# Kernel optimization log

Measured on AMD Instinct MI355X. Metric: run time of the kernel, lower is better.

The kernel has to match this reference:

```python
import jax, jax.numpy as jnp
import numpy as np

VOCAB = 10000
HID = 256
BATCH = 32
STEPS = 256


def setup_inputs() -> dict:
    key = jax.random.key(0)
    k1, k2, k3, k4 = jax.random.split(key, 4)
    # glorot-uniform style scaling
    s_xh = np.sqrt(6.0 / (VOCAB + HID)).astype(np.float32)
    s_hh = np.sqrt(6.0 / (HID + HID)).astype(np.float32)
    s_d = np.sqrt(6.0 / (HID + VOCAB)).astype(np.float32)
    return {
        "tokens": jax.random.randint(k1, (BATCH, STEPS), 0, VOCAB, dtype=jnp.int32),
        "W_xh": jax.random.uniform(k2, (VOCAB, HID), jnp.float32, -s_xh, s_xh),
        "W_hh": jax.random.uniform(k3, (HID, HID), jnp.float32, -s_hh, s_hh),
        "b_h": jnp.zeros((HID,), jnp.float32),
        "W_d": jax.random.uniform(k4, (HID, VOCAB), jnp.float32, -s_d, s_d),
        "b_d": jnp.zeros((VOCAB,), jnp.float32),
        "h0": jnp.zeros((BATCH, HID), jnp.float32),
    }


def reference(tokens, W_xh, W_hh, b_h, W_d, b_d, h0):
    # call(): X = one_hot(transpose(tokens), vocab)  -> time-major [T, B, V]
    # one_hot(x) @ W_xh is exactly a row gather from W_xh (same math, efficient form)
    xw = W_xh[jnp.transpose(tokens)]  # [T, B, H]

    # SimpleRNNCell: h_t = tanh(x_t @ W_xh + h_{t-1} @ W_hh + b)
    def step(h, xt):
        h_new = jnp.tanh(xt + h @ W_hh + b_h)
        return h_new, h_new

    state, Y = jax.lax.scan(step, h0, xw)  # Y: [T, B, H], state: [B, H]

    # Dense over flattened sequence outputs -> [T*B, vocab]
    output = Y.reshape(-1, Y.shape[-1]) @ W_d + b_d
    return output, state
```

## Files before the change

### kernel.cpp

```cpp
#include <hip/hip_runtime.h>
#include <hip/hip_bf16.h>

#define VOCAB 10000
#define HID 256
#define BATCH 32
#define STEPS 256
#define MROWS (STEPS * BATCH)

typedef __bf16 bf16x8 __attribute__((ext_vector_type(8)));
typedef float f32x4 __attribute__((ext_vector_type(4)));

template <int CTRL>
static __device__ __forceinline__ float dpp_add(float s) {
    int t = __builtin_amdgcn_update_dpp(
        0, __builtin_bit_cast(int, s), CTRL, 0xf, 0xf, true);
    return s + __builtin_bit_cast(float, t);
}
#define DPP_XOR1 0xB1
#define DPP_XOR2 0x4E

static __device__ __forceinline__ float swz4_add(float s) {
    int t = __builtin_amdgcn_ds_swizzle(__builtin_bit_cast(int, s), 0x101F);
    return s + __builtin_bit_cast(float, t);
}

__global__ void transpose_wd_kernel(const float* __restrict__ Wd,
                                    __hip_bfloat16* __restrict__ WdT) {
    __shared__ __hip_bfloat16 tile[64][68];
    const int n0 = blockIdx.x * 64;
    const int k0 = blockIdx.y * 64;
    const int tid = threadIdx.x;
    const int lane = tid & 63;
    const int w = tid >> 6;

#pragma unroll
    for (int i = 0; i < 16; ++i) {
        int k = w * 16 + i;
        int n = lane;
        float v = (n0 + n < VOCAB) ? Wd[(size_t)(k0 + k) * VOCAB + n0 + n] : 0.f;
        tile[n][k] = __float2bfloat16(v);
    }
    __syncthreads();
#pragma unroll
    for (int i = 0; i < 16; ++i) {
        int n = w * 16 + i;
        int k = lane;
        if (n0 + n < VOCAB)
            WdT[(size_t)(n0 + n) * HID + k0 + k] = tile[n][k];
    }
}

#define HSEG 36

__global__ __launch_bounds__(1024)
__attribute__((amdgpu_waves_per_eu(4, 4)))
void rnn_kernel(const int* __restrict__ tokens, const float* __restrict__ Wxh,
                const float* __restrict__ Whh, const float* __restrict__ bh,
                const float* __restrict__ h0, __hip_bfloat16* __restrict__ ybf,
                float* __restrict__ state_out) {
    const int b = blockIdx.x;
    const int tid = threadIdx.x;
    const int cg = tid >> 3;
    const int q = tid & 7;
    const int c0 = cg * 2;

    __shared__ alignas(16) float hseg[2][8][HSEG];

    float w0[32], w1[32];
    {
        const float* wp = Whh + (size_t)(q * 32) * HID + c0;
#pragma unroll
        for (int i = 0; i < 32; ++i) {
            w0[i] = wp[(size_t)i * HID];
            w1[i] = wp[(size_t)i * HID + 1];
        }
    }

    const float bj0 = bh[c0];
    const float bj1 = bh[c0 + 1];
    const int* trow = tokens + b * STEPS;

    if (q == 0) {
        hseg[0][c0 >> 5][c0 & 31] = h0[b * HID + c0];
        hseg[0][c0 >> 5][(c0 & 31) + 1] = h0[b * HID + c0 + 1];
    }

    float2 xv = *reinterpret_cast<const float2*>(&Wxh[(size_t)trow[0] * HID + c0]);
    __syncthreads();

    float hn0 = 0.f, hn1 = 0.f;
    int cur = 0;
    for (int t = 0; t < STEPS; ++t) {
#pragma unroll
        for (int i = 0; i < 32; ++i) {
            asm volatile("" : "+v"(w0[i]), "+v"(w1[i]));
        }

        int ti = (t + 1 < STEPS) ? t + 1 : STEPS - 1;
        float2 xn = *reinterpret_cast<const float2*>(
            &Wxh[(size_t)trow[ti] * HID + c0]);

        const float* hb = &hseg[cur][q][0];
        float s0 = 0.f, s1 = 0.f;
#pragma unroll
        for (int j4 = 0; j4 < 8; ++j4) {
            float4 hv = *reinterpret_cast<const float4*>(&hb[j4 * 4]);
            s0 += hv.x * w0[j4 * 4 + 0] + hv.y * w0[j4 * 4 + 1] +
                  hv.z * w0[j4 * 4 + 2] + hv.w * w0[j4 * 4 + 3];
            s1 += hv.x * w1[j4 * 4 + 0] + hv.y * w1[j4 * 4 + 1] +
                  hv.z * w1[j4 * 4 + 2] + hv.w * w1[j4 * 4 + 3];
        }
        s0 = dpp_add<DPP_XOR1>(s0);  s1 = dpp_add<DPP_XOR1>(s1);
        s0 = dpp_add<DPP_XOR2>(s0);  s1 = dpp_add<DPP_XOR2>(s1);
        s0 = swz4_add(s0);           s1 = swz4_add(s1);

        float z0 = xv.x + bj0 + s0;
        float z1 = xv.y + bj1 + s1;
        float e0 = __expf(2.f * z0);
        float e1 = __expf(2.f * z1);
        hn0 = 1.f - 2.f / (e0 + 1.f);
        hn1 = 1.f - 2.f / (e1 + 1.f);

        if (q == 0) {
            float2 hp = make_float2(hn0, hn1);
            *reinterpret_cast<float2*>(&hseg[cur ^ 1][c0 >> 5][c0 & 31]) = hp;
        } else if (q == 1) {
            __hip_bfloat162 yp;
            yp.x = __float2bfloat16(hn0);
            yp.y = __float2bfloat16(hn1);
            *reinterpret_cast<__hip_bfloat162*>(
                &ybf[(size_t)t * (BATCH * HID) + b * HID + c0]) = yp;
        }

        __syncthreads();
        cur ^= 1;
        xv = xn;
    }
    if (q == 1) {
        state_out[b * HID + c0] = hn0;
        state_out[b * HID + c0 + 1] = hn1;
    }
}

__global__ __launch_bounds__(256)
void gemm_kernel(const __hip_bfloat16* __restrict__ A,
                 const __hip_bfloat16* __restrict__ BT,
                 const float* __restrict__ bd,
                 float* __restrict__ C) {
    const int m0 = blockIdx.x * 128;
    const int n0 = blockIdx.y * 128;
    const int tid = threadIdx.x;
    const int lane = tid & 63;
    const int wv = tid >> 6;
    const int wr = wv >> 1;
    const int wc = wv & 1;
    const int r15 = lane & 15;
    const int g = lane >> 4;

    __shared__ alignas(16) __hip_bfloat16 As[128][264];

#pragma unroll
    for (int c = 0; c < 16; ++c) {
        int chunk = c * 256 + tid;
        int row = chunk >> 5;
        int cc = chunk & 31;
        bf16x8 av = *reinterpret_cast<const bf16x8*>(
            &A[(size_t)(m0 + row) * HID + cc * 8]);
        *reinterpret_cast<bf16x8*>(&As[row][cc * 8]) = av;
    }
    __syncthreads();

    const __hip_bfloat16* brow[4];
    bool bok[4];
#pragma unroll
    for (int n = 0; n < 4; ++n) {
        int rn = n0 + wc * 64 + n * 16 + r15;
        bok[n] = rn < VOCAB;
        brow[n] = BT + (size_t)(bok[n] ? rn : 0) * HID;
    }
    bf16x8 bzero;
#pragma unroll
    for (int e = 0; e < 8; ++e) bzero[e] = (__bf16)0.f;

    f32x4 acc[4][4] = {};
    bf16x8 bcur[4];
#pragma unroll
    for (int n = 0; n < 4; ++n)
        bcur[n] = bok[n] ? *reinterpret_cast<const bf16x8*>(&brow[n][g * 8])
                         : bzero;

    for (int kk8 = 0; kk8 < 8; ++kk8) {
        bf16x8 bnext[4];
        if (kk8 < 7) {
            int off = (kk8 + 1) * 32 + g * 8;
#pragma unroll
            for (int n = 0; n < 4; ++n)
                bnext[n] = bok[n]
                    ? *reinterpret_cast<const bf16x8*>(&brow[n][off])
                    : bzero;
        }
        bf16x8 af[4];
#pragma unroll
        for (int m = 0; m < 4; ++m)
            af[m] = *reinterpret_cast<const bf16x8*>(
                &As[wr * 64 + m * 16 + r15][kk8 * 32 + g * 8]);
#pragma unroll
        for (int m = 0; m < 4; ++m)
#pragma unroll
            for (int n = 0; n < 4; ++n)
                acc[m][n] = __builtin_amdgcn_mfma_f32_16x16x32_bf16(
                    bcur[n], af[m], acc[m][n], 0, 0, 0);
        if (kk8 < 7) {
#pragma unroll
            for (int n = 0; n < 4; ++n) bcur[n] = bnext[n];
        }
    }

#pragma unroll
    for (int m = 0; m < 4; ++m) {
        int row = m0 + wr * 64 + m * 16 + r15;
#pragma unroll
        for (int n = 0; n < 4; ++n) {
            int cb = n0 + wc * 64 + n * 16;
            if (cb + 15 < VOCAB) {
                int col = cb + g * 4;
                float4 bv = *reinterpret_cast<const float4*>(&bd[col]);
                f32x4 v = acc[m][n];
                v[0] += bv.x; v[1] += bv.y; v[2] += bv.z; v[3] += bv.w;
                *reinterpret_cast<f32x4*>(&C[(size_t)row * VOCAB + col]) = v;
            }
        }
    }
}

extern "C" void kernel_launch(void* const* d_in, const int* in_sizes, int n_in,
                              void* d_out, int out_size, void* d_ws, size_t ws_size,
                              hipStream_t stream) {
    const int* tokens  = (const int*)d_in[0];
    const float* Wxh   = (const float*)d_in[1];
    const float* Whh   = (const float*)d_in[2];
    const float* bh    = (const float*)d_in[3];
    const float* Wd    = (const float*)d_in[4];
    const float* bd    = (const float*)d_in[5];
    const float* h0    = (const float*)d_in[6];

    float* out = (float*)d_out;
    float* state_out = out + (size_t)MROWS * VOCAB;

    __hip_bfloat16* ybf = (__hip_bfloat16*)d_ws;
    __hip_bfloat16* wdt = (__hip_bfloat16*)((char*)d_ws + (size_t)MROWS * HID * 2);

    hipLaunchKernelGGL(transpose_wd_kernel, dim3(157, 4), dim3(256), 0, stream,
                       Wd, wdt);
    hipLaunchKernelGGL(rnn_kernel, dim3(BATCH), dim3(1024), 0, stream,
                       tokens, Wxh, Whh, bh, h0, ybf, state_out);
    hipLaunchKernelGGL(gemm_kernel, dim3(64, 79), dim3(256), 0, stream,
                       ybf, wdt, bd, out);
}
```

Baseline: 429.5 us.

## Halve RNN block to 512 threads with four columns per thread group

The recurrent kernel now runs 512 threads per batch row, each 8-lane group owning four hidden columns instead of two, so each thread holds 128 weight registers. A new kernel transposes W_hh into the workspace so those weights load as contiguous float4 rows. The intent is to cut the per-step barrier cost and the number of waves that synchronise, at the price of more FMA work per thread, higher register pressure, and an extra kernel launch.

```diff
diff --git a/kernel.cpp b/kernel.cpp
--- a/kernel.cpp
+++ b/kernel.cpp
@@ -9,6 +9,7 @@
 
 typedef __bf16 bf16x8 __attribute__((ext_vector_type(8)));
 typedef float f32x4 __attribute__((ext_vector_type(4)));
+typedef unsigned short u16x4 __attribute__((ext_vector_type(4)));
 
 template <int CTRL>
 static __device__ __forceinline__ float dpp_add(float s) {
@@ -50,95 +51,123 @@
     }
 }
 
+__global__ void transpose_whh_kernel(const float* __restrict__ Whh,
+                                     float* __restrict__ WhhT) {
+    __shared__ float tile[64][65];
+    const int j0 = blockIdx.x * 64;
+    const int k0 = blockIdx.y * 64;
+    const int tid = threadIdx.x;
+    const int lane = tid & 63;
+    const int w = tid >> 6;
+
+#pragma unroll
+    for (int i = 0; i < 16; ++i) {
+        int k = w * 16 + i;
+        tile[lane][k] = Whh[(size_t)(k0 + k) * HID + j0 + lane];
+    }
+    __syncthreads();
+#pragma unroll
+    for (int i = 0; i < 16; ++i) {
+        int j = w * 16 + i;
+        WhhT[(size_t)(j0 + j) * HID + k0 + lane] = tile[j][lane];
+    }
+}
+
 #define HSEG 36
 
-__global__ __launch_bounds__(1024)
-__attribute__((amdgpu_waves_per_eu(4, 4)))
+__global__ __launch_bounds__(512, 2)
+__attribute__((amdgpu_waves_per_eu(2, 2)))
 void rnn_kernel(const int* __restrict__ tokens, const float* __restrict__ Wxh,
-                const float* __restrict__ Whh, const float* __restrict__ bh,
+                const float* __restrict__ WhhT, const float* __restrict__ bh,
                 const float* __restrict__ h0, __hip_bfloat16* __restrict__ ybf,
                 float* __restrict__ state_out) {
     const int b = blockIdx.x;
     const int tid = threadIdx.x;
     const int cg = tid >> 3;
     const int q = tid & 7;
-    const int c0 = cg * 2;
+    const int c0 = cg * 4;
 
     __shared__ alignas(16) float hseg[2][8][HSEG];
 
-    float w0[32], w1[32];
-    {
-        const float* wp = Whh + (size_t)(q * 32) * HID + c0;
-#pragma unroll
-        for (int i = 0; i < 32; ++i) {
-            w0[i] = wp[(size_t)i * HID];
-            w1[i] = wp[(size_t)i * HID + 1];
-        }
-    }
-
-    const float bj0 = bh[c0];
-    const float bj1 = bh[c0 + 1];
+    float w[4][32];
+#pragma unroll
+    for (int c = 0; c < 4; ++c) {
+        const float4* wp = reinterpret_cast<const float4*>(
+            WhhT + (size_t)(c0 + c) * HID + q * 32);
+#pragma unroll
+        for (int i4 = 0; i4 < 8; ++i4) {
+            float4 v = wp[i4];
+            w[c][i4 * 4 + 0] = v.x;
+            w[c][i4 * 4 + 1] = v.y;
+            w[c][i4 * 4 + 2] = v.z;
+            w[c][i4 * 4 + 3] = v.w;
+        }
+    }
+
+    const float4 bj = *reinterpret_cast<const float4*>(&bh[c0]);
     const int* trow = tokens + b * STEPS;
 
     if (q == 0) {
-        hseg[0][c0 >> 5][c0 & 31] = h0[b * HID + c0];
-        hseg[0][c0 >> 5][(c0 & 31) + 1] = h0[b * HID + c0 + 1];
-    }
-
-    float2 xv = *reinterpret_cast<const float2*>(&Wxh[(size_t)trow[0] * HID + c0]);
-    __syncthreads();
-
-    float hn0 = 0.f, hn1 = 0.f;
+        *reinterpret_cast<float4*>(&hseg[0][c0 >> 5][c0 & 31]) =
+            *reinterpret_cast<const float4*>(&h0[b * HID + c0]);
+    }
+
+    float4 xv = *reinterpret_cast<const float4*>(&Wxh[(size_t)trow[0] * HID + c0]);
+    __syncthreads();
+
+    float hn[4] = {0.f, 0.f, 0.f, 0.f};
     int cur = 0;
     for (int t = 0; t < STEPS; ++t) {
-#pragma unroll
-        for (int i = 0; i < 32; ++i) {
-            asm volatile("" : "+v"(w0[i]), "+v"(w1[i]));
-        }
-
         int ti = (t + 1 < STEPS) ? t + 1 : STEPS - 1;
-        float2 xn = *reinterpret_cast<const float2*>(
+        float4 xn = *reinterpret_cast<const float4*>(
             &Wxh[(size_t)trow[ti] * HID + c0]);
 
         const float* hb = &hseg[cur][q][0];
-        float s0 = 0.f, s1 = 0.f;
+        float s[4] = {0.f, 0.f, 0.f, 0.f};
 #pragma unroll
         for (int j4 = 0; j4 < 8; ++j4) {
             float4 hv = *reinterpret_cast<const float4*>(&hb[j4 * 4]);
-            s0 += hv.x * w0[j4 * 4 + 0] + hv.y * w0[j4 * 4 + 1] +
-                  hv.z * w0[j4 * 4 + 2] + hv.w * w0[j4 * 4 + 3];
-            s1 += hv.x * w1[j4 * 4 + 0] + hv.y * w1[j4 * 4 + 1] +
-                  hv.z * w1[j4 * 4 + 2] + hv.w * w1[j4 * 4 + 3];
-        }
-        s0 = dpp_add<DPP_XOR1>(s0);  s1 = dpp_add<DPP_XOR1>(s1);
-        s0 = dpp_add<DPP_XOR2>(s0);  s1 = dpp_add<DPP_XOR2>(s1);
-        s0 = swz4_add(s0);           s1 = swz4_add(s1);
-
-        float z0 = xv.x + bj0 + s0;
-        float z1 = xv.y + bj1 + s1;
-        float e0 = __expf(2.f * z0);
-        float e1 = __expf(2.f * z1);
-        hn0 = 1.f - 2.f / (e0 + 1.f);
-        hn1 = 1.f - 2.f / (e1 + 1.f);
+#pragma unroll
+            for (int c = 0; c < 4; ++c)
+                s[c] += hv.x * w[c][j4 * 4 + 0] + hv.y * w[c][j4 * 4 + 1] +
+                        hv.z * w[c][j4 * 4 + 2] + hv.w * w[c][j4 * 4 + 3];
+        }
+#pragma unroll
+        for (int c = 0; c < 4; ++c) {
+            s[c] = dpp_add<DPP_XOR1>(s[c]);
+            s[c] = dpp_add<DPP_XOR2>(s[c]);
+            s[c] = swz4_add(s[c]);
+        }
+
+        const float x4[4] = {xv.x, xv.y, xv.z, xv.w};
+        const float b4[4] = {bj.x, bj.y, bj.z, bj.w};
+#pragma unroll
+        for (int c = 0; c < 4; ++c) {
+            float z = x4[c] + b4[c] + s[c];
+            float e = __expf(2.f * z);
+            hn[c] = 1.f - 2.f / (e + 1.f);
+        }
 
         if (q == 0) {
-            float2 hp = make_float2(hn0, hn1);
-            *reinterpret_cast<float2*>(&hseg[cur ^ 1][c0 >> 5][c0 & 31]) = hp;
+            *reinterpret_cast<float4*>(&hseg[cur ^ 1][c0 >> 5][c0 & 31]) =
+                make_float4(hn[0], hn[1], hn[2], hn[3]);
         } else if (q == 1) {
-            __hip_bfloat162 yp;
-            yp.x = __float2bfloat16(hn0);
-            yp.y = __float2bfloat16(hn1);
-            *reinterpret_cast<__hip_bfloat162*>(
-                &ybf[(size_t)t * (BATCH * HID) + b * HID + c0]) = yp;
+            u16x4 yv;
+#pragma unroll
+            for (int c = 0; c < 4; ++c)
+                yv[c] = __builtin_bit_cast(unsigned short,
+                                           __float2bfloat16(hn[c]));
+            *reinterpret_cast<u16x4*>(
+                &ybf[(size_t)t * (BATCH * HID) + b * HID + c0]) = yv;
         }
 
         __syncthreads();
         cur ^= 1;
         xv = xn;
     }
-    if (q == 1) {
-        state_out[b * HID + c0] = hn0;
-        state_out[b * HID + c0 + 1] = hn1;
+    if (q == 2) {
+        *reinterpret_cast<float4*>(&state_out[b * HID + c0]) =
+            make_float4(hn[0], hn[1], hn[2], hn[3]);
     }
 }
 
@@ -247,13 +276,17 @@
     float* out = (float*)d_out;
     float* state_out = out + (size_t)MROWS * VOCAB;
 
-    __hip_bfloat16* ybf = (__hip_bfloat16*)d_ws;
-    __hip_bfloat16* wdt = (__hip_bfloat16*)((char*)d_ws + (size_t)MROWS * HID * 2);
-
+    char* wsb = (char*)d_ws;
+    __hip_bfloat16* ybf = (__hip_bfloat16*)wsb;
+    __hip_bfloat16* wdt = (__hip_bfloat16*)(wsb + (size_t)MROWS * HID * 2);
+    float* whhT = (float*)(wsb + (size_t)MROWS * HID * 2 + (size_t)VOCAB * HID * 2);
+
+    hipLaunchKernelGGL(transpose_whh_kernel, dim3(4, 4), dim3(256), 0, stream,
+                       Whh, whhT);
     hipLaunchKernelGGL(transpose_wd_kernel, dim3(157, 4), dim3(256), 0, stream,
                        Wd, wdt);
-    hipLaunchKernelGGL(rnn_kernel, dim3(BATCH), dim3(1024), 0, stream,
-                       tokens, Wxh, Whh, bh, h0, ybf, state_out);
+    hipLaunchKernelGGL(rnn_kernel, dim3(BATCH), dim3(512), 0, stream,
+                       tokens, Wxh, whhT, bh, h0, ybf, state_out);
     hipLaunchKernelGGL(gemm_kernel, dim3(64, 79), dim3(256), 0, stream,
                        ybf, wdt, bd, out);
 }
```

New measurement: 423.1 us. Within noise of the previous version (-1.5%).
